# Optimization experiments

Hardware: AMD Instinct MI355X
Metric: run time of the kernel (lower is better)

Reference implementation:

```python
import jax, jax.numpy as jnp
import numpy as np

B, N, D_MEM, D_HID = 64, 65536, 1024, 1024


def setup_inputs() -> dict:
    key = jax.random.key(0)
    k1, k2, k3 = jax.random.split(key, 3)
    memory_bank = jax.random.normal(k1, (N, D_MEM), dtype=jnp.float32)
    decoder_state = jax.random.normal(k2, (B, D_HID), dtype=jnp.float32)
    # nn.Linear(memory_bank_size -> hidden_size, bias=False): weight [D_HID, D_MEM]
    W = jax.random.normal(k3, (D_HID, D_MEM), dtype=jnp.float32) / np.sqrt(D_MEM)
    # ragged tree sizes summing exactly to N (concrete, built on host)
    rng = np.random.default_rng(0)
    lens = rng.integers(512, 1536, size=B).astype(np.float64)
    lens = np.maximum(1, np.floor(lens * N / lens.sum()).astype(np.int64))
    lens[-1] += N - lens.sum()
    return {
        "memory_bank": memory_bank,
        "decoder_state": decoder_state,
        "W": W,
        "tree_node_num_lst": jnp.asarray(lens, dtype=jnp.int64),
    }


def reference(memory_bank, decoder_state, W, tree_node_num_lst):
    # segment id per node: tree index it belongs to (total_repeat_length keeps it jit-able)
    n_total = memory_bank.shape[0]
    batch = decoder_state.shape[0]
    seg = jnp.repeat(jnp.arange(batch), tree_node_num_lst, total_repeat_length=n_total)  # [N]
    # memory_project: one big GEMM instead of per-tree launches
    enc = memory_bank @ W.T                                  # [N, D_HID]
    # per-node score = <decoder_state[tree], enc[node]>
    scores = jnp.sum(enc * decoder_state[seg], axis=-1)      # [N]
    # segment (per-tree) stable softmax
    m = jax.ops.segment_max(scores, seg, num_segments=batch)  # [B]
    e = jnp.exp(scores - m[seg])                              # [N]
    z = jax.ops.segment_sum(e, seg, num_segments=batch)       # [B]
    attn = e / z[seg]                                         # [N]
    # context = attn-weighted sum of raw memory bank per tree
    context = jax.ops.segment_sum(attn[:, None] * memory_bank, seg, num_segments=batch)  # [B, D_MEM]
    return context
```

## Files before the change

kernel.cpp:

```cpp
#include <hip/hip_runtime.h>
#include <hip/hip_bf16.h>
#include <math.h>

#define B_TREES 64
#define N_NODES 65536
#define D 1024
#define D4 (D/4)
#define PIECE 16
#define MAXP (N_NODES/PIECE + B_TREES)

__global__ void setup_kernel(const int* __restrict__ lens32,
                             int* __restrict__ off, int* __restrict__ pbase,
                             int* __restrict__ pseg, int* __restrict__ pstart,
                             int* __restrict__ plen) {
    __shared__ int sh_off[B_TREES + 1];
    __shared__ int sh_pb[B_TREES + 1];

    const int t = threadIdx.x;
    if (t < 64) {
        const int lane = t;
        int l32 = lens32[lane];
        int s = l32;
        #pragma unroll
        for (int o = 32; o > 0; o >>= 1) s += __shfl_xor(s, o, 64);
        const bool is32 = (s == N_NODES);
        int len = is32 ? l32 : (int)(((const long long*)lens32)[lane]);
        int scan = len;
        #pragma unroll
        for (int o = 1; o < 64; o <<= 1) {
            int u = __shfl_up(scan, o, 64);
            if (lane >= o) scan += u;
        }
        int pc = (len + PIECE - 1) / PIECE;
        int pscan = pc;
        #pragma unroll
        for (int o = 1; o < 64; o <<= 1) {
            int u = __shfl_up(pscan, o, 64);
            if (lane >= o) pscan += u;
        }
        sh_off[lane + 1] = scan;
        sh_pb[lane + 1]  = pscan;
        if (lane == 0) { sh_off[0] = 0; sh_pb[0] = 0; }
        off[lane + 1]   = scan;
        pbase[lane + 1] = pscan;
        if (lane == 0) { off[0] = 0; pbase[0] = 0; }
    }
    __syncthreads();

    const int total = sh_pb[B_TREES];
    for (int p = t; p < total; p += 256) {
        int lo = 0, hi = B_TREES - 1;
        while (lo < hi) {
            int mid = (lo + hi + 1) >> 1;
            if (sh_pb[mid] <= p) lo = mid; else hi = mid - 1;
        }
        const int i  = p - sh_pb[lo];
        const int st = sh_off[lo] + i * PIECE;
        pseg[p]   = lo;
        pstart[p] = st;
        plen[p]   = min(PIECE, sh_off[lo + 1] - st);
    }
}

__global__ void v_kernel(const float* __restrict__ ds, const float* __restrict__ W,
                         float* __restrict__ v) {
    const int m  = blockIdx.x * 256 + threadIdx.x;
    const int b0 = blockIdx.y * 4;
    const int h0 = blockIdx.z * 128;
    float acc[4] = {0.f, 0.f, 0.f, 0.f};
    for (int h = h0; h < h0 + 128; ++h) {
        float wv = W[h * D + m];
        #pragma unroll
        for (int j = 0; j < 4; ++j)
            acc[j] += ds[(b0 + j) * D + h] * wv;
    }
    #pragma unroll
    for (int j = 0; j < 4; ++j)
        atomicAdd(&v[(b0 + j) * D + m], acc[j]);
}

__global__ __launch_bounds__(256) void fused_kernel(
        const float4* __restrict__ mb, const float4* __restrict__ v,
        const int* __restrict__ pseg, const int* __restrict__ pstart,
        const int* __restrict__ plen, const int* __restrict__ pbase,
        float* __restrict__ pm, float* __restrict__ pz, float4* __restrict__ pctx) {
    const int wave = threadIdx.x >> 6;
    const int lane = threadIdx.x & 63;
    const int p    = blockIdx.x * 4 + wave;
    if (p >= pbase[B_TREES]) return;

    const int seg = pseg[p];
    const int s0  = pstart[p];
    const int ln  = plen[p];

    const float4* vrow = v + (size_t)seg * D4;
    const float4 v0 = vrow[lane], v1 = vrow[64 + lane],
                 v2 = vrow[128 + lane], v3 = vrow[192 + lane];

    float4 a0 = make_float4(0.f,0.f,0.f,0.f), a1 = a0, a2 = a0, a3 = a0;
    float rm = -INFINITY, rz = 0.f;

    const float4* base = mb + (size_t)s0 * D4;

    if (ln == PIECE) {
        #pragma unroll 2
        for (int i = 0; i < PIECE; i += 2) {
            const float4* rA = base + (size_t)i * D4;
            const float4* rB = rA + D4;
            const float4 A0 = rA[lane],       A1 = rA[64 + lane],
                         A2 = rA[128 + lane], A3 = rA[192 + lane];
            const float4 B0 = rB[lane],       B1 = rB[64 + lane],
                         B2 = rB[128 + lane], B3 = rB[192 + lane];
            float dA = (A0.x*v0.x + A0.y*v0.y + A0.z*v0.z + A0.w*v0.w)
                     + (A1.x*v1.x + A1.y*v1.y + A1.z*v1.z + A1.w*v1.w)
                     + (A2.x*v2.x + A2.y*v2.y + A2.z*v2.z + A2.w*v2.w)
                     + (A3.x*v3.x + A3.y*v3.y + A3.z*v3.z + A3.w*v3.w);
            float dB = (B0.x*v0.x + B0.y*v0.y + B0.z*v0.z + B0.w*v0.w)
                     + (B1.x*v1.x + B1.y*v1.y + B1.z*v1.z + B1.w*v1.w)
                     + (B2.x*v2.x + B2.y*v2.y + B2.z*v2.z + B2.w*v2.w)
                     + (B3.x*v3.x + B3.y*v3.y + B3.z*v3.z + B3.w*v3.w);
            #pragma unroll
            for (int o = 32; o > 0; o >>= 1) {
                dA += __shfl_xor(dA, o, 64);
                dB += __shfl_xor(dB, o, 64);
            }
            const float nm = fmaxf(rm, fmaxf(dA, dB));
            const float sc = __expf(rm - nm);
            const float wA = __expf(dA - nm);
            const float wB = __expf(dB - nm);
            a0.x = a0.x*sc + wA*A0.x + wB*B0.x; a0.y = a0.y*sc + wA*A0.y + wB*B0.y;
            a0.z = a0.z*sc + wA*A0.z + wB*B0.z; a0.w = a0.w*sc + wA*A0.w + wB*B0.w;
            a1.x = a1.x*sc + wA*A1.x + wB*B1.x; a1.y = a1.y*sc + wA*A1.y + wB*B1.y;
            a1.z = a1.z*sc + wA*A1.z + wB*B1.z; a1.w = a1.w*sc + wA*A1.w + wB*B1.w;
            a2.x = a2.x*sc + wA*A2.x + wB*B2.x; a2.y = a2.y*sc + wA*A2.y + wB*B2.y;
            a2.z = a2.z*sc + wA*A2.z + wB*B2.z; a2.w = a2.w*sc + wA*A2.w + wB*B2.w;
            a3.x = a3.x*sc + wA*A3.x + wB*B3.x; a3.y = a3.y*sc + wA*A3.y + wB*B3.y;
            a3.z = a3.z*sc + wA*A3.z + wB*B3.z; a3.w = a3.w*sc + wA*A3.w + wB*B3.w;
            rz = rz*sc + wA + wB;
            rm = nm;
        }
    } else {
        for (int i = 0; i < ln; ++i) {
            const float4* mrow = base + (size_t)i * D4;
            const float4 m0 = mrow[lane],       m1 = mrow[64 + lane],
                         m2 = mrow[128 + lane], m3 = mrow[192 + lane];
            float d = (m0.x*v0.x + m0.y*v0.y + m0.z*v0.z + m0.w*v0.w)
                    + (m1.x*v1.x + m1.y*v1.y + m1.z*v1.z + m1.w*v1.w)
                    + (m2.x*v2.x + m2.y*v2.y + m2.z*v2.z + m2.w*v2.w)
                    + (m3.x*v3.x + m3.y*v3.y + m3.z*v3.z + m3.w*v3.w);
            #pragma unroll
            for (int o = 32; o > 0; o >>= 1) d += __shfl_xor(d, o, 64);
            const float nm = fmaxf(rm, d);
            const float sc = __expf(rm - nm);
            const float w  = __expf(d - nm);
            a0.x = a0.x*sc + w*m0.x; a0.y = a0.y*sc + w*m0.y;
            a0.z = a0.z*sc + w*m0.z; a0.w = a0.w*sc + w*m0.w;
            a1.x = a1.x*sc + w*m1.x; a1.y = a1.y*sc + w*m1.y;
            a1.z = a1.z*sc + w*m1.z; a1.w = a1.w*sc + w*m1.w;
            a2.x = a2.x*sc + w*m2.x; a2.y = a2.y*sc + w*m2.y;
            a2.z = a2.z*sc + w*m2.z; a2.w = a2.w*sc + w*m2.w;
            a3.x = a3.x*sc + w*m3.x; a3.y = a3.y*sc + w*m3.y;
            a3.z = a3.z*sc + w*m3.z; a3.w = a3.w*sc + w*m3.w;
            rz = rz*sc + w;
            rm = nm;
        }
    }

    if (lane == 0) { pm[p] = rm; pz[p] = rz; }
    float4* o = pctx + (size_t)p * D4;
    o[lane] = a0; o[64 + lane] = a1; o[128 + lane] = a2; o[192 + lane] = a3;
}

__global__ void finalize_kernel(const int* __restrict__ pbase,
                                const float* __restrict__ pm, const float* __restrict__ pz,
                                const float4* __restrict__ pctx, float4* __restrict__ out) {
    const int b  = blockIdx.x;
    const int t  = threadIdx.x;
    const int q0 = pbase[b], q1 = pbase[b + 1];

    float mb_ = -INFINITY;
    for (int q = q0; q < q1; ++q) mb_ = fmaxf(mb_, pm[q]);
    float zb = 0.f;
    for (int q = q0; q < q1; ++q) zb += pz[q] * __expf(pm[q] - mb_);
    const float inv = 1.f / zb;

    float4 acc = make_float4(0.f,0.f,0.f,0.f);
    for (int q = q0; q < q1; ++q) {
        const float s = __expf(pm[q] - mb_);
        const float4 c = pctx[(size_t)q * D4 + t];
        acc.x += s * c.x; acc.y += s * c.y; acc.z += s * c.z; acc.w += s * c.w;
    }
    acc.x *= inv; acc.y *= inv; acc.z *= inv; acc.w *= inv;
    out[(size_t)b * D4 + t] = acc;
}

extern "C" void kernel_launch(void* const* d_in, const int* in_sizes, int n_in,
                              void* d_out, int out_size, void* d_ws, size_t ws_size,
                              hipStream_t stream) {
    const float* mb   = (const float*)d_in[0];
    const float* ds   = (const float*)d_in[1];
    const float* W    = (const float*)d_in[2];
    const int*   lens = (const int*)d_in[3];
    float*       out  = (float*)d_out;

    char* ws = (char*)d_ws;
    int*   off    = (int*)(ws + 0);
    int*   pbase  = (int*)(ws + 512);
    float* v      = (float*)(ws + 1024);
    int*   pseg   = (int*)(ws + 1024 + 262144);
    int*   pstart = (int*)(ws + 1024 + 262144 + 32768);
    int*   plen   = (int*)(ws + 1024 + 262144 + 65536);
    float* pm     = (float*)(ws + 1024 + 262144 + 98304);
    float* pz     = (float*)(ws + 1024 + 262144 + 131072);
    float4* pctx  = (float4*)(ws + 1024 + 262144 + 163840);

    hipMemsetAsync(v, 0, 64 * D * sizeof(float), stream);

    setup_kernel<<<1, 256, 0, stream>>>(lens, off, pbase, pseg, pstart, plen);

    {
        dim3 grid(4, 16, 8);
        v_kernel<<<grid, 256, 0, stream>>>(ds, W, v);
    }

    fused_kernel<<<(MAXP + 3) / 4, 256, 0, stream>>>(
        (const float4*)mb, (const float4*)v, pseg, pstart, plen, pbase,
        pm, pz, pctx);

    finalize_kernel<<<B_TREES, 256, 0, stream>>>(
        pbase, pm, pz, pctx, (float4*)out);
}
```

Baseline: 437.8 us.

## Merge setup and v projection into one kernel, unroll fused loop by four rows

Merges the segment-setup kernel and the decoder-state projection kernel into one launch. The projection now computes each output with a full-length dot product per thread, which removes the memset and the atomics. The main streaming kernel now processes four memory rows per iteration instead of two, giving more loads in flight and fewer rescale steps in the online softmax. The tradeoffs are a less parallel projection (256 blocks each looping over 1024 elements) and higher register pressure in the fused loop.

```diff
diff --git a/kernel.cpp b/kernel.cpp
--- a/kernel.cpp
+++ b/kernel.cpp
@@ -9,74 +9,81 @@
 #define PIECE 16
 #define MAXP (N_NODES/PIECE + B_TREES)
 
-__global__ void setup_kernel(const int* __restrict__ lens32,
-                             int* __restrict__ off, int* __restrict__ pbase,
-                             int* __restrict__ pseg, int* __restrict__ pstart,
-                             int* __restrict__ plen) {
-    __shared__ int sh_off[B_TREES + 1];
-    __shared__ int sh_pb[B_TREES + 1];
-
+__device__ __forceinline__ float dot4(const float4 a, const float4 b) {
+    return a.x*b.x + a.y*b.y + a.z*b.z + a.w*b.w;
+}
+__device__ __forceinline__ void upd4(float4& a, const float sc,
+                                     const float w0, const float4 x0,
+                                     const float w1, const float4 x1,
+                                     const float w2, const float4 x2,
+                                     const float w3, const float4 x3) {
+    a.x = a.x*sc + w0*x0.x + w1*x1.x + w2*x2.x + w3*x3.x;
+    a.y = a.y*sc + w0*x0.y + w1*x1.y + w2*x2.y + w3*x3.y;
+    a.z = a.z*sc + w0*x0.z + w1*x1.z + w2*x2.z + w3*x3.z;
+    a.w = a.w*sc + w0*x0.w + w1*x1.w + w2*x2.w + w3*x3.w;
+}
+
+__global__ __launch_bounds__(256) void combo_kernel(
+        const float* __restrict__ ds, const float* __restrict__ W,
+        const int* __restrict__ lens32,
+        float* __restrict__ v, int* __restrict__ pbase,
+        int* __restrict__ pseg, int* __restrict__ pstart,
+        int* __restrict__ plen) {
     const int t = threadIdx.x;
-    if (t < 64) {
-        const int lane = t;
-        int l32 = lens32[lane];
-        int s = l32;
-        #pragma unroll
-        for (int o = 32; o > 0; o >>= 1) s += __shfl_xor(s, o, 64);
-        const bool is32 = (s == N_NODES);
-        int len = is32 ? l32 : (int)(((const long long*)lens32)[lane]);
-        int scan = len;
-        #pragma unroll
-        for (int o = 1; o < 64; o <<= 1) {
-            int u = __shfl_up(scan, o, 64);
-            if (lane >= o) scan += u;
-        }
-        int pc = (len + PIECE - 1) / PIECE;
-        int pscan = pc;
-        #pragma unroll
-        for (int o = 1; o < 64; o <<= 1) {
-            int u = __shfl_up(pscan, o, 64);
-            if (lane >= o) pscan += u;
-        }
-        sh_off[lane + 1] = scan;
-        sh_pb[lane + 1]  = pscan;
-        if (lane == 0) { sh_off[0] = 0; sh_pb[0] = 0; }
-        off[lane + 1]   = scan;
-        pbase[lane + 1] = pscan;
-        if (lane == 0) { off[0] = 0; pbase[0] = 0; }
-    }
-    __syncthreads();
-
-    const int total = sh_pb[B_TREES];
-    for (int p = t; p < total; p += 256) {
-        int lo = 0, hi = B_TREES - 1;
-        while (lo < hi) {
-            int mid = (lo + hi + 1) >> 1;
-            if (sh_pb[mid] <= p) lo = mid; else hi = mid - 1;
-        }
-        const int i  = p - sh_pb[lo];
-        const int st = sh_off[lo] + i * PIECE;
-        pseg[p]   = lo;
-        pstart[p] = st;
-        plen[p]   = min(PIECE, sh_off[lo + 1] - st);
-    }
-}
-
-__global__ void v_kernel(const float* __restrict__ ds, const float* __restrict__ W,
-                         float* __restrict__ v) {
-    const int m  = blockIdx.x * 256 + threadIdx.x;
-    const int b0 = blockIdx.y * 4;
-    const int h0 = blockIdx.z * 128;
-    float acc[4] = {0.f, 0.f, 0.f, 0.f};
-    for (int h = h0; h < h0 + 128; ++h) {
-        float wv = W[h * D + m];
-        #pragma unroll
-        for (int j = 0; j < 4; ++j)
-            acc[j] += ds[(b0 + j) * D + h] * wv;
-    }
-    #pragma unroll
-    for (int j = 0; j < 4; ++j)
-        atomicAdd(&v[(b0 + j) * D + m], acc[j]);
+    const int m = blockIdx.x * 256 + t;
+    const int b = blockIdx.y;
+    const float* dsrow = ds + (size_t)b * D;
+    float acc = 0.f;
+    #pragma unroll 8
+    for (int h = 0; h < D; ++h)
+        acc += dsrow[h] * W[(size_t)h * D + m];
+    v[(size_t)b * D + m] = acc;
+
+    if (blockIdx.x == 0 && blockIdx.y == 0) {
+        __shared__ int sh_off[B_TREES + 1];
+        __shared__ int sh_pb[B_TREES + 1];
+        if (t < 64) {
+            const int lane = t;
+            int l32 = lens32[lane];
+            int s = l32;
+            #pragma unroll
+            for (int o = 32; o > 0; o >>= 1) s += __shfl_xor(s, o, 64);
+            const bool is32 = (s == N_NODES);
+            int len = is32 ? l32 : (int)(((const long long*)lens32)[lane]);
+            int scan = len;
+            #pragma unroll
+            for (int o = 1; o < 64; o <<= 1) {
+                int u = __shfl_up(scan, o, 64);
+                if (lane >= o) scan += u;
+            }
+            int pc = (len + PIECE - 1) / PIECE;
+            int pscan = pc;
+            #pragma unroll
+            for (int o = 1; o < 64; o <<= 1) {
+                int u = __shfl_up(pscan, o, 64);
+                if (lane >= o) pscan += u;
+            }
+            sh_off[lane + 1] = scan;
+            sh_pb[lane + 1]  = pscan;
+            if (lane == 0) { sh_off[0] = 0; sh_pb[0] = 0; }
+            pbase[lane + 1] = pscan;
+            if (lane == 0) pbase[0] = 0;
+        }
+        __syncthreads();
+        const int total = sh_pb[B_TREES];
+        for (int p = t; p < total; p += 256) {
+            int lo = 0, hi = B_TREES - 1;
+            while (lo < hi) {
+                int mid = (lo + hi + 1) >> 1;
+                if (sh_pb[mid] <= p) lo = mid; else hi = mid - 1;
+            }
+            const int i  = p - sh_pb[lo];
+            const int st = sh_off[lo] + i * PIECE;
+            pseg[p]   = lo;
+            pstart[p] = st;
+            plen[p]   = min(PIECE, sh_off[lo + 1] - st);
+        }
+    }
 }
 
 __global__ __launch_bounds__(256) void fused_kernel(
@@ -103,40 +110,36 @@
     const float4* base = mb + (size_t)s0 * D4;
 
     if (ln == PIECE) {
-        #pragma unroll 2
-        for (int i = 0; i < PIECE; i += 2) {
-            const float4* rA = base + (size_t)i * D4;
-            const float4* rB = rA + D4;
-            const float4 A0 = rA[lane],       A1 = rA[64 + lane],
-                         A2 = rA[128 + lane], A3 = rA[192 + lane];
-            const float4 B0 = rB[lane],       B1 = rB[64 + lane],
-                         B2 = rB[128 + lane], B3 = rB[192 + lane];
-            float dA = (A0.x*v0.x + A0.y*v0.y + A0.z*v0.z + A0.w*v0.w)
-                     + (A1.x*v1.x + A1.y*v1.y + A1.z*v1.z + A1.w*v1.w)
-                     + (A2.x*v2.x + A2.y*v2.y + A2.z*v2.z + A2.w*v2.w)
-                     + (A3.x*v3.x + A3.y*v3.y + A3.z*v3.z + A3.w*v3.w);
-            float dB = (B0.x*v0.x + B0.y*v0.y + B0.z*v0.z + B0.w*v0.w)
-                     + (B1.x*v1.x + B1.y*v1.y + B1.z*v1.z + B1.w*v1.w)
-                     + (B2.x*v2.x + B2.y*v2.y + B2.z*v2.z + B2.w*v2.w)
-                     + (B3.x*v3.x + B3.y*v3.y + B3.z*v3.z + B3.w*v3.w);
+        #pragma unroll 1
+        for (int g = 0; g < PIECE; g += 4) {
+            const float4* r0 = base + (size_t)g * D4;
+            const float4* r1 = r0 + D4;
+            const float4* r2 = r0 + 2 * D4;
+            const float4* r3 = r0 + 3 * D4;
+            const float4 x00=r0[lane], x01=r0[64+lane], x02=r0[128+lane], x03=r0[192+lane];
+            const float4 x10=r1[lane], x11=r1[64+lane], x12=r1[128+lane], x13=r1[192+lane];
+            const float4 x20=r2[lane], x21=r2[64+lane], x22=r2[128+lane], x23=r2[192+lane];
+            const float4 x30=r3[lane], x31=r3[64+lane], x32=r3[128+lane], x33=r3[192+lane];
+            float d0 = (dot4(x00,v0)+dot4(x01,v1)) + (dot4(x02,v2)+dot4(x03,v3));
+            float d1 = (dot4(x10,v0)+dot4(x11,v1)) + (dot4(x12,v2)+dot4(x13,v3));
+            float d2 = (dot4(x20,v0)+dot4(x21,v1)) + (dot4(x22,v2)+dot4(x23,v3));
+            float d3 = (dot4(x30,v0)+dot4(x31,v1)) + (dot4(x32,v2)+dot4(x33,v3));
             #pragma unroll
             for (int o = 32; o > 0; o >>= 1) {
-                dA += __shfl_xor(dA, o, 64);
-                dB += __shfl_xor(dB, o, 64);
-            }
-            const float nm = fmaxf(rm, fmaxf(dA, dB));
+                d0 += __shfl_xor(d0, o, 64);
+                d1 += __shfl_xor(d1, o, 64);
+                d2 += __shfl_xor(d2, o, 64);
+                d3 += __shfl_xor(d3, o, 64);
+            }
+            const float nm = fmaxf(rm, fmaxf(fmaxf(d0, d1), fmaxf(d2, d3)));
             const float sc = __expf(rm - nm);
-            const float wA = __expf(dA - nm);
-            const float wB = __expf(dB - nm);
-            a0.x = a0.x*sc + wA*A0.x + wB*B0.x; a0.y = a0.y*sc + wA*A0.y + wB*B0.y;
-            a0.z = a0.z*sc + wA*A0.z + wB*B0.z; a0.w = a0.w*sc + wA*A0.w + wB*B0.w;
-            a1.x = a1.x*sc + wA*A1.x + wB*B1.x; a1.y = a1.y*sc + wA*A1.y + wB*B1.y;
-            a1.z = a1.z*sc + wA*A1.z + wB*B1.z; a1.w = a1.w*sc + wA*A1.w + wB*B1.w;
-            a2.x = a2.x*sc + wA*A2.x + wB*B2.x; a2.y = a2.y*sc + wA*A2.y + wB*B2.y;
-            a2.z = a2.z*sc + wA*A2.z + wB*B2.z; a2.w = a2.w*sc + wA*A2.w + wB*B2.w;
-            a3.x = a3.x*sc + wA*A3.x + wB*B3.x; a3.y = a3.y*sc + wA*A3.y + wB*B3.y;
-            a3.z = a3.z*sc + wA*A3.z + wB*B3.z; a3.w = a3.w*sc + wA*A3.w + wB*B3.w;
-            rz = rz*sc + wA + wB;
+            const float w0 = __expf(d0 - nm), w1 = __expf(d1 - nm);
+            const float w2 = __expf(d2 - nm), w3 = __expf(d3 - nm);
+            upd4(a0, sc, w0, x00, w1, x10, w2, x20, w3, x30);
+            upd4(a1, sc, w0, x01, w1, x11, w2, x21, w3, x31);
+            upd4(a2, sc, w0, x02, w1, x12, w2, x22, w3, x32);
+            upd4(a3, sc, w0, x03, w1, x13, w2, x23, w3, x33);
+            rz = rz*sc + (w0 + w1) + (w2 + w3);
             rm = nm;
         }
     } else {
@@ -144,10 +147,7 @@
             const float4* mrow = base + (size_t)i * D4;
             const float4 m0 = mrow[lane],       m1 = mrow[64 + lane],
                          m2 = mrow[128 + lane], m3 = mrow[192 + lane];
-            float d = (m0.x*v0.x + m0.y*v0.y + m0.z*v0.z + m0.w*v0.w)
-                    + (m1.x*v1.x + m1.y*v1.y + m1.z*v1.z + m1.w*v1.w)
-                    + (m2.x*v2.x + m2.y*v2.y + m2.z*v2.z + m2.w*v2.w)
-                    + (m3.x*v3.x + m3.y*v3.y + m3.z*v3.z + m3.w*v3.w);
+            float d = (dot4(m0,v0)+dot4(m1,v1)) + (dot4(m2,v2)+dot4(m3,v3));
             #pragma unroll
             for (int o = 32; o > 0; o >>= 1) d += __shfl_xor(d, o, 64);
             const float nm = fmaxf(rm, d);
@@ -204,8 +204,7 @@
     float*       out  = (float*)d_out;
 
     char* ws = (char*)d_ws;
-    int*   off    = (int*)(ws + 0);
-    int*   pbase  = (int*)(ws + 512);
+    int*   pbase  = (int*)(ws + 0);
     float* v      = (float*)(ws + 1024);
     int*   pseg   = (int*)(ws + 1024 + 262144);
     int*   pstart = (int*)(ws + 1024 + 262144 + 32768);
@@ -214,13 +213,10 @@
     float* pz     = (float*)(ws + 1024 + 262144 + 131072);
     float4* pctx  = (float4*)(ws + 1024 + 262144 + 163840);
 
-    hipMemsetAsync(v, 0, 64 * D * sizeof(float), stream);
-
-    setup_kernel<<<1, 256, 0, stream>>>(lens, off, pbase, pseg, pstart, plen);
-
     {
-        dim3 grid(4, 16, 8);
-        v_kernel<<<grid, 256, 0, stream>>>(ds, W, v);
+        dim3 grid(4, 64);
+        combo_kernel<<<grid, 256, 0, stream>>>(ds, W, lens, v,
+                                               pbase, pseg, pstart, plen);
     }
 
     fused_kernel<<<(MAXP + 3) / 4, 256, 0, stream>>>(
```

After: 479.8 us. 9.6% more time.
